# Performance work log

Measured on AMD Instinct MI355X. Metric: run time of the kernel, lower is better.

## Reference

```python
import jax, jax.numpy as jnp
import numpy as np

H = 128          # hidden_size
EF = 2           # expansion_factor
E = H * EF       # expanded hidden size
K = 4            # conv kernel size
R = 8            # dt_rank = ceil(128/16)
L = 2            # num_layers
BATCH = 2
SEQ = 1024
EPS = 1e-5


def rmsnorm(x, w):
    return x * jax.lax.rsqrt(jnp.mean(x * x, axis=-1, keepdims=True) + EPS) * w


def causal_conv1d(x, w, b):
    # x: (b, l, E); w: (E, 1, K) depthwise; left-pad K-1 => causal, output len l
    xt = jnp.transpose(x, (0, 2, 1))  # (b, E, l)
    out = jax.lax.conv_general_dilated(
        xt, w, window_strides=(1,), padding=[(K - 1, 0)],
        dimension_numbers=("NCH", "OIH", "NCH"), feature_group_count=E)
    out = out + b[None, :, None]
    return jnp.transpose(out, (0, 2, 1))


def sscan(xc, delta, A, Bm, Cm, Dp):
    # xc, delta: (b,l,E); A: (E,n); Bm, Cm: (b,l,n); Dp: (E,)
    deltaA = jnp.exp(jnp.einsum('bld,dn->bldn', delta, A))          # (b,l,E,n)
    deltaBx = jnp.einsum('bld,bln,bld->bldn', delta, Bm, xc)        # (b,l,E,n)

    def step(h, inp):
        dA_t, dBx_t, C_t = inp           # (b,E,n), (b,E,n), (b,n)
        h = dA_t * h + dBx_t
        y = jnp.einsum('bdn,bn->bd', h, C_t)
        return h, y

    b = xc.shape[0]
    h0 = jnp.zeros((b, E, A.shape[1]), dtype=xc.dtype)
    _, ys = jax.lax.scan(
        step, h0,
        (jnp.transpose(deltaA, (1, 0, 2, 3)),
         jnp.transpose(deltaBx, (1, 0, 2, 3)),
         jnp.transpose(Cm, (1, 0, 2))))
    y = jnp.transpose(ys, (1, 0, 2))     # (b,l,E)
    return y + Dp * xc


def mamba_block(x, in_w, in_b, out_w, out_b, pl_w, pl_b, dt_w, dt_b,
                conv_w, conv_b, A_log, Dp):
    xz = x @ in_w + in_b                 # (b,l,2E)
    xc, skip = jnp.split(xz, [E], axis=-1)
    xc = jax.nn.silu(causal_conv1d(xc, conv_w, conv_b))
    # ssm
    A = -jnp.exp(A_log)                  # (E,H)
    dbc = xc @ pl_w + pl_b               # (b,l,R+2H)
    delta, Bm, Cm = jnp.split(dbc, [R, R + H], axis=-1)
    delta = jax.nn.softplus(delta @ dt_w + dt_b)   # (b,l,E)
    y = sscan(xc, delta, A, Bm, Cm, Dp)
    y = y * jax.nn.silu(skip)
    return y @ out_w + out_b


def forward(x, in_w, in_b, out_w, out_b, pl_w, pl_b, dt_w, dt_b,
            conv_w, conv_b, A_log, Dp, norm_w, final_norm_w):
    for i in range(L):
        x = mamba_block(rmsnorm(x, norm_w[i]), in_w[i], in_b[i], out_w[i],
                        out_b[i], pl_w[i], pl_b[i], dt_w[i], dt_b[i],
                        conv_w[i], conv_b[i], A_log[i], Dp[i]) + x
    return rmsnorm(x, final_norm_w)


def setup_inputs() -> dict:
    key = jax.random.key(0)
    ks = jax.random.split(key, 12)
    s = 0.02
    x = jax.random.normal(ks[0], (BATCH, SEQ, H), dtype=jnp.float32)
    in_w = jax.random.normal(ks[1], (L, H, 2 * E)) * s
    in_b = jnp.zeros((L, 2 * E))
    out_w = jax.random.normal(ks[2], (L, E, H)) * s
    out_b = jnp.zeros((L, H))
    pl_w = jax.random.normal(ks[3], (L, E, R + 2 * H)) * s
    pl_b = jnp.zeros((L, R + 2 * H))
    dt_w = jax.random.normal(ks[4], (L, R, E)) * s
    dt_b = jnp.zeros((L, E))
    conv_w = jax.random.normal(ks[5], (L, E, 1, K)) * (1.0 / np.sqrt(K))
    conv_b = jnp.zeros((L, E))
    A_log = jnp.broadcast_to(jnp.log(jnp.arange(1, H + 1, dtype=jnp.float32)),
                             (L, E, H))
    Dp = jnp.ones((L, E))
    norm_w = jnp.ones((L, H))
    final_norm_w = jnp.ones((H,))
    return {"x": x, "in_w": in_w, "in_b": in_b, "out_w": out_w,
            "out_b": out_b, "pl_w": pl_w, "pl_b": pl_b, "dt_w": dt_w,
            "dt_b": dt_b, "conv_w": conv_w, "conv_b": conv_b,
            "A_log": A_log, "Dp": Dp, "norm_w": norm_w,
            "final_norm_w": final_norm_w}


def reference(x, in_w, in_b, out_w, out_b, pl_w, pl_b, dt_w, dt_b,
              conv_w, conv_b, A_log, Dp, norm_w, final_norm_w):
    return forward(x, in_w, in_b, out_w, out_b, pl_w, pl_b, dt_w, dt_b,
                   conv_w, conv_b, A_log, Dp, norm_w, final_norm_w)
```

## Files before the change

kernel.cpp:

```cpp
#include <hip/hip_runtime.h>
#include <hip/hip_bf16.h>

#define HH 128
#define EE 256
#define KK 4
#define RR 8
#define LL 2
#define BB 2
#define SS 1024
#define BT (BB*SS)
#define NJ (RR+2*HH)
#define GG 16
#define CH (SS/GG)
#define EPS 1e-5f
#define LOG2E 1.44269504088896f

__device__ __forceinline__ float silu_f(float v) {
    return v / (1.0f + __expf(-v));
}

__global__ __launch_bounds__(512) void k_norm_inproj(
    const float* __restrict__ xres, const float* __restrict__ inw,
    const float* __restrict__ inb, const float* __restrict__ nw,
    float* __restrict__ xz)
{
    __shared__ float xn[16][128];
    const int bt0 = blockIdx.x * 16;
    const int tid = threadIdx.x;
    {
        const int t = tid >> 5, g = tid & 31;
        const float4 xv = *(const float4*)(xres + (bt0 + t) * HH + g * 4);
        float ss = xv.x*xv.x + xv.y*xv.y + xv.z*xv.z + xv.w*xv.w;
        #pragma unroll
        for (int m = 16; m >= 1; m >>= 1) ss += __shfl_xor(ss, m);
        const float rs = rsqrtf(ss * (1.0f / HH) + EPS);
        const float4 wv = *(const float4*)(nw + g * 4);
        float4 o;
        o.x = xv.x * rs * wv.x; o.y = xv.y * rs * wv.y;
        o.z = xv.z * rs * wv.z; o.w = xv.w * rs * wv.w;
        *(float4*)(&xn[t][g * 4]) = o;
    }
    __syncthreads();
    const int j = tid;
    float acc[16];
    const float bj = inb[j];
    #pragma unroll
    for (int t = 0; t < 16; t++) acc[t] = bj;
    float w0n = inw[0*512 + j], w1n = inw[1*512 + j];
    float w2n = inw[2*512 + j], w3n = inw[3*512 + j];
    for (int k4 = 0; k4 < 32; k4++) {
        const float w0 = w0n, w1 = w1n, w2 = w2n, w3 = w3n;
        if (k4 < 31) {
            const int k = (k4 + 1) * 4;
            w0n = inw[(k+0)*512 + j]; w1n = inw[(k+1)*512 + j];
            w2n = inw[(k+2)*512 + j]; w3n = inw[(k+3)*512 + j];
        }
        const int k = k4 * 4;
        #pragma unroll
        for (int t = 0; t < 16; t++) {
            const float4 xv = *(const float4*)(&xn[t][k]);
            acc[t] += w0*xv.x + w1*xv.y + w2*xv.z + w3*xv.w;
        }
    }
    #pragma unroll
    for (int t = 0; t < 16; t++) xz[(bt0 + t) * 512 + j] = acc[t];
}

__global__ __launch_bounds__(256) void k_conv(
    const float* __restrict__ xz, const float* __restrict__ cw,
    const float* __restrict__ cb, float* __restrict__ xcT)
{
    const int e = threadIdx.x;
    const int tile = blockIdx.x;
    const int b = tile >> 6;
    const int t0 = (tile & 63) * 16;
    const float w0 = cw[e*4+0], w1 = cw[e*4+1], w2 = cw[e*4+2], w3 = cw[e*4+3];
    const float bias = cb[e];
    const float* xp = xz + (size_t)(b * SS) * 512 + e;
    float xm3 = (t0 >= 3) ? xp[(t0-3)*512] : 0.0f;
    float xm2 = (t0 >= 2) ? xp[(t0-2)*512] : 0.0f;
    float xm1 = (t0 >= 1) ? xp[(t0-1)*512] : 0.0f;
    float* orow = xcT + (size_t)e * BT + b * SS + t0;
    for (int jq = 0; jq < 4; jq++) {
        const int t = t0 + jq * 4;
        float4 ob; float v;
        const float x0 = xp[(t+0)*512];
        v = bias + w3*x0 + w2*xm1 + w1*xm2 + w0*xm3; ob.x = silu_f(v);
        const float x1 = xp[(t+1)*512];
        v = bias + w3*x1 + w2*x0 + w1*xm1 + w0*xm2;  ob.y = silu_f(v);
        const float x2 = xp[(t+2)*512];
        v = bias + w3*x2 + w2*x1 + w1*x0 + w0*xm1;   ob.z = silu_f(v);
        const float x3 = xp[(t+3)*512];
        v = bias + w3*x3 + w2*x2 + w1*x1 + w0*x0;    ob.w = silu_f(v);
        *(float4*)(orow + jq * 4) = ob;
        xm3 = x1; xm2 = x2; xm1 = x3;
    }
}

__global__ __launch_bounds__(320) void k_plproj(
    const float* __restrict__ xcT, const float* __restrict__ plw,
    const float* __restrict__ plb, float* __restrict__ dtrows,
    float* __restrict__ BC4)
{
    __shared__ float xs[8][256];
    const int bt0 = blockIdx.x * 8;
    const int tid = threadIdx.x;
    if (tid < 256) {
        const int e = tid;
        const float* p = xcT + (size_t)e * BT + bt0;
        const float4 a = *(const float4*)(p);
        const float4 c = *(const float4*)(p + 4);
        xs[0][e] = a.x; xs[1][e] = a.y; xs[2][e] = a.z; xs[3][e] = a.w;
        xs[4][e] = c.x; xs[5][e] = c.y; xs[6][e] = c.z; xs[7][e] = c.w;
    }
    __syncthreads();
    if (tid >= NJ) return;
    const int j = tid;
    float acc[8];
    const float bj = plb[j];
    #pragma unroll
    for (int t = 0; t < 8; t++) acc[t] = bj;
    float w0n = plw[0*NJ + j], w1n = plw[1*NJ + j];
    float w2n = plw[2*NJ + j], w3n = plw[3*NJ + j];
    for (int e4 = 0; e4 < 64; e4++) {
        const float w0 = w0n, w1 = w1n, w2 = w2n, w3 = w3n;
        if (e4 < 63) {
            const int e = (e4 + 1) * 4;
            w0n = plw[(e+0)*NJ + j]; w1n = plw[(e+1)*NJ + j];
            w2n = plw[(e+2)*NJ + j]; w3n = plw[(e+3)*NJ + j];
        }
        const int e = e4 * 4;
        #pragma unroll
        for (int t = 0; t < 8; t++) {
            const float4 xv = *(const float4*)(&xs[t][e]);
            acc[t] += w0*xv.x + w1*xv.y + w2*xv.z + w3*xv.w;
        }
    }
    if (j < RR) {
        float* orow = dtrows + (size_t)j * BT + bt0;
        *(float4*)(orow)     = make_float4(acc[0], acc[1], acc[2], acc[3]);
        *(float4*)(orow + 4) = make_float4(acc[4], acc[5], acc[6], acc[7]);
    } else {
        const int isC = (j >= RR + HH);
        const int nn = isC ? (j - RR - HH) : (j - RR);
        const int tq0 = bt0 >> 2;
        float* p0 = BC4 + ((size_t)tq0 * 128 + nn) * 8 + (isC ? 4 : 0);
        *(float4*)p0 = make_float4(acc[0], acc[1], acc[2], acc[3]);
        float* p1 = BC4 + ((size_t)(tq0 + 1) * 128 + nn) * 8 + (isC ? 4 : 0);
        *(float4*)p1 = make_float4(acc[4], acc[5], acc[6], acc[7]);
    }
}

__global__ __launch_bounds__(256) void k_delta(
    const float* __restrict__ dtrows, const float* __restrict__ dtw,
    const float* __restrict__ dtb, const float* __restrict__ xcT,
    float* __restrict__ deltaT, float* __restrict__ sT,
    float* __restrict__ dsum)
{
    const int e = blockIdx.x >> 3;
    const int bt = (blockIdx.x & 7) * 256 + threadIdx.x;
    float d = dtb[e];
    #pragma unroll
    for (int r = 0; r < RR; r++) d += dtw[r*EE + e] * dtrows[(size_t)r * BT + bt];
    float sp;
    if (d > 15.0f) sp = d;
    else sp = log1pf(__expf(d));
    const float xc = xcT[(size_t)e * BT + bt];
    deltaT[(size_t)e * BT + bt] = sp;
    sT[(size_t)e * BT + bt] = sp * xc;
    float cs = sp;
    #pragma unroll
    for (int m = 1; m <= 32; m <<= 1) cs += __shfl_xor(cs, m);
    if ((threadIdx.x & 63) == 0) {
        const int b = bt >> 10;
        const int g = (bt & 1023) >> 6;
        dsum[(b * EE + e) * GG + g] = cs;
    }
}

__global__ __launch_bounds__(128, 4) void k_scan_local(
    const float* __restrict__ BC4, const float* __restrict__ deltaT,
    const float* __restrict__ sT, const float* __restrict__ Alog,
    float* __restrict__ yT, float* __restrict__ hchain)
{
    __shared__ float part[2][16][68];
    __shared__ float ybuf[2][CH];
    const int blk = blockIdx.x;
    const int wgid = (blk & 7) * 512 + (blk >> 3);
    const int eq = wgid & 127;
    const int r0 = wgid >> 7;
    const int b = r0 >> 4;
    const int g = r0 & 15;
    const int e0 = eq * 2;
    const int n = threadIdx.x;
    const int t0 = g * CH;

    float An0 = -__expf(Alog[(e0+0) * HH + n]) * LOG2E;
    float An1 = -__expf(Alog[(e0+1) * HH + n]) * LOG2E;
    float h0 = 0.0f, h1 = 0.0f;
    const float* bc = BC4 + ((size_t)((b * 256 + g * 16) * 128 + n)) * 8;
    const float* dr0 = deltaT + (size_t)(e0+0) * BT + b * SS + t0;
    const float* dr1 = deltaT + (size_t)(e0+1) * BT + b * SS + t0;
    const float* sr0 = sT + (size_t)(e0+0) * BT + b * SS + t0;
    const float* sr1 = sT + (size_t)(e0+1) * BT + b * SS + t0;

    float4 pB = *(const float4*)(bc);
    float4 pC = *(const float4*)(bc + 4);
    float4 pd0 = *(const float4*)dr0, pd1 = *(const float4*)dr1;
    float4 ps0 = *(const float4*)sr0, ps1 = *(const float4*)sr1;

    const int tl = n >> 3, jj = n & 7;
    for (int sc = 0; sc < 4; sc++) {
        #pragma unroll
        for (int q = 0; q < 4; q++) {
            const int qq = sc * 4 + q;
            const float4 cB = pB, cC = pC;
            const float4 cd0 = pd0, cd1 = pd1, cs0 = ps0, cs1 = ps1;
            if (qq < 15) {
                const size_t off = (size_t)(qq + 1) * 1024;
                pB = *(const float4*)(bc + off);
                pC = *(const float4*)(bc + off + 4);
                const int t = (qq + 1) * 4;
                pd0 = *(const float4*)(dr0 + t); pd1 = *(const float4*)(dr1 + t);
                ps0 = *(const float4*)(sr0 + t); ps1 = *(const float4*)(sr1 + t);
            }
            float a;
            a = exp2f(cd0.x*An0); h0 = a*h0 + cs0.x*cB.x; part[0][q*4+0][n] = h0*cC.x;
            a = exp2f(cd0.y*An0); h0 = a*h0 + cs0.y*cB.y; part[0][q*4+1][n] = h0*cC.y;
            a = exp2f(cd0.z*An0); h0 = a*h0 + cs0.z*cB.z; part[0][q*4+2][n] = h0*cC.z;
            a = exp2f(cd0.w*An0); h0 = a*h0 + cs0.w*cB.w; part[0][q*4+3][n] = h0*cC.w;
            a = exp2f(cd1.x*An1); h1 = a*h1 + cs1.x*cB.x; part[1][q*4+0][n] = h1*cC.x;
            a = exp2f(cd1.y*An1); h1 = a*h1 + cs1.y*cB.y; part[1][q*4+1][n] = h1*cC.y;
            a = exp2f(cd1.z*An1); h1 = a*h1 + cs1.z*cB.z; part[1][q*4+2][n] = h1*cC.z;
            a = exp2f(cd1.w*An1); h1 = a*h1 + cs1.w*cB.w; part[1][q*4+3][n] = h1*cC.w;
        }
        __syncthreads();
        #pragma unroll
        for (int ee = 0; ee < 2; ee++) {
            float s0 = 0, s1 = 0, s2 = 0, s3 = 0;
            #pragma unroll
            for (int i = 0; i < 4; i++) {
                const float4 p = *(const float4*)(&part[ee][tl][jj*16 + i*4]);
                s0 += p.x; s1 += p.y; s2 += p.z; s3 += p.w;
            }
            float r = (s0 + s1) + (s2 + s3);
            r += __shfl_xor(r, 1); r += __shfl_xor(r, 2); r += __shfl_xor(r, 4);
            if (jj == 0) ybuf[ee][sc*16 + tl] = r;
        }
        __syncthreads();
    }
    {
        const int ee = n >> 6, tt = n & 63;
        yT[(size_t)(e0 + ee) * BT + b * SS + t0 + tt] = ybuf[ee][tt];
    }
    hchain[(size_t)(((b * EE + e0 + 0) * GG) + g) * 128 + n] = h0;
    hchain[(size_t)(((b * EE + e0 + 1) * GG) + g) * 128 + n] = h1;
}

__global__ __launch_bounds__(128) void k_scan_combine(
    const float* __restrict__ Alog, const float* __restrict__ dsum,
    float* __restrict__ hchain)
{
    const int be = blockIdx.x;
    const int e = be & 255;
    const int n = threadIdx.x;
    const float An = -__expf(Alog[e * HH + n]) * LOG2E;
    float h = 0.0f;
    for (int g = 0; g < GG; g++) {
        float* p = hchain + (size_t)(be * GG + g) * 128 + n;
        const float he = *p;
        *p = h;
        const float ds = dsum[be * GG + g];
        h = exp2f(An * ds) * h + he;
    }
}

__global__ __launch_bounds__(128, 4) void k_scan_fix(
    const float* __restrict__ BC4, const float* __restrict__ deltaT,
    const float* __restrict__ Alog, const float* __restrict__ hchain,
    float* __restrict__ yT)
{
    __shared__ float part[2][16][68];
    __shared__ float ybuf[2][CH];
    const int blk = blockIdx.x;
    const int wgid = (blk & 7) * 480 + (blk >> 3);
    const int eq = wgid & 127;
    const int r0 = wgid >> 7;
    const int b = r0 / 15;
    const int g = 1 + (r0 % 15);
    const int e0 = eq * 2;
    const int n = threadIdx.x;
    const int t0 = g * CH;

    const float An0 = -__expf(Alog[(e0+0) * HH + n]) * LOG2E;
    const float An1 = -__expf(Alog[(e0+1) * HH + n]) * LOG2E;
    const float w0 = hchain[(size_t)(((b * EE + e0 + 0) * GG) + g) * 128 + n];
    const float w1 = hchain[(size_t)(((b * EE + e0 + 1) * GG) + g) * 128 + n];
    float D0 = 0.0f, D1 = 0.0f;
    const float* bc = BC4 + ((size_t)((b * 256 + g * 16) * 128 + n)) * 8;
    const float* dr0 = deltaT + (size_t)(e0+0) * BT + b * SS + t0;
    const float* dr1 = deltaT + (size_t)(e0+1) * BT + b * SS + t0;

    float4 pC = *(const float4*)(bc + 4);
    float4 pd0 = *(const float4*)dr0, pd1 = *(const float4*)dr1;

    const int tl = n >> 3, jj = n & 7;
    for (int sc = 0; sc < 4; sc++) {
        #pragma unroll
        for (int q = 0; q < 4; q++) {
            const int qq = sc * 4 + q;
            const float4 cC = pC;
            const float4 cd0 = pd0, cd1 = pd1;
            if (qq < 15) {
                const size_t off = (size_t)(qq + 1) * 1024;
                pC = *(const float4*)(bc + off + 4);
                const int t = (qq + 1) * 4;
                pd0 = *(const float4*)(dr0 + t); pd1 = *(const float4*)(dr1 + t);
            }
            D0 += cd0.x; part[0][q*4+0][n] = exp2f(An0*D0) * w0 * cC.x;
            D0 += cd0.y; part[0][q*4+1][n] = exp2f(An0*D0) * w0 * cC.y;
            D0 += cd0.z; part[0][q*4+2][n] = exp2f(An0*D0) * w0 * cC.z;
            D0 += cd0.w; part[0][q*4+3][n] = exp2f(An0*D0) * w0 * cC.w;
            D1 += cd1.x; part[1][q*4+0][n] = exp2f(An1*D1) * w1 * cC.x;
            D1 += cd1.y; part[1][q*4+1][n] = exp2f(An1*D1) * w1 * cC.y;
            D1 += cd1.z; part[1][q*4+2][n] = exp2f(An1*D1) * w1 * cC.z;
            D1 += cd1.w; part[1][q*4+3][n] = exp2f(An1*D1) * w1 * cC.w;
        }
        __syncthreads();
        #pragma unroll
        for (int ee = 0; ee < 2; ee++) {
            float s0 = 0, s1 = 0, s2 = 0, s3 = 0;
            #pragma unroll
            for (int i = 0; i < 4; i++) {
                const float4 p = *(const float4*)(&part[ee][tl][jj*16 + i*4]);
                s0 += p.x; s1 += p.y; s2 += p.z; s3 += p.w;
            }
            float r = (s0 + s1) + (s2 + s3);
            r += __shfl_xor(r, 1); r += __shfl_xor(r, 2); r += __shfl_xor(r, 4);
            if (jj == 0) ybuf[ee][sc*16 + tl] = r;
        }
        __syncthreads();
    }
    {
        const int ee = n >> 6, tt = n & 63;
        yT[(size_t)(e0 + ee) * BT + b * SS + t0 + tt] += ybuf[ee][tt];
    }
}

__global__ __launch_bounds__(256) void k_gate_outproj(
    const float* __restrict__ yT, const float* __restrict__ xcT,
    const float* __restrict__ xz, const float* __restrict__ Dp,
    const float* __restrict__ ow, const float* __restrict__ ob,
    float* __restrict__ xres)
{
    __shared__ float gs[16][256];
    __shared__ float part2[16][128];
    const int bt0 = blockIdx.x * 16;
    const int tid = threadIdx.x;
    {
        const int e = tid;
        const float dp = Dp[e];
        const float* yp = yT + (size_t)e * BT + bt0;
        const float* xp = xcT + (size_t)e * BT + bt0;
        #pragma unroll
        for (int tq = 0; tq < 4; tq++) {
            const float4 y4 = *(const float4*)(yp + tq * 4);
            const float4 x4 = *(const float4*)(xp + tq * 4);
            float sk;
            sk = xz[(size_t)(bt0 + tq*4 + 0) * 512 + 256 + e];
            gs[tq*4+0][e] = (y4.x + dp * x4.x) * silu_f(sk);
            sk = xz[(size_t)(bt0 + tq*4 + 1) * 512 + 256 + e];
            gs[tq*4+1][e] = (y4.y + dp * x4.y) * silu_f(sk);
            sk = xz[(size_t)(bt0 + tq*4 + 2) * 512 + 256 + e];
            gs[tq*4+2][e] = (y4.z + dp * x4.z) * silu_f(sk);
            sk = xz[(size_t)(bt0 + tq*4 + 3) * 512 + 256 + e];
            gs[tq*4+3][e] = (y4.w + dp * x4.w) * silu_f(sk);
        }
    }
    __syncthreads();
    const int j = tid & 127;
    const int kh = tid >> 7;
    float acc[16];
    #pragma unroll
    for (int t = 0; t < 16; t++) acc[t] = 0.0f;
    const int eb = kh * 128;
    float w0n = ow[(eb+0)*HH + j], w1n = ow[(eb+1)*HH + j];
    float w2n = ow[(eb+2)*HH + j], w3n = ow[(eb+3)*HH + j];
    for (int e4 = 0; e4 < 32; e4++) {
        const float w0 = w0n, w1 = w1n, w2 = w2n, w3 = w3n;
        if (e4 < 31) {
            const int e = eb + (e4 + 1) * 4;
            w0n = ow[(e+0)*HH + j]; w1n = ow[(e+1)*HH + j];
            w2n = ow[(e+2)*HH + j]; w3n = ow[(e+3)*HH + j];
        }
        const int e = eb + e4 * 4;
        #pragma unroll
        for (int t = 0; t < 16; t++) {
            const float4 g4 = *(const float4*)(&gs[t][e]);
            acc[t] += w0*g4.x + w1*g4.y + w2*g4.z + w3*g4.w;
        }
    }
    if (kh == 1) {
        #pragma unroll
        for (int t = 0; t < 16; t++) part2[t][j] = acc[t];
    }
    __syncthreads();
    if (kh == 0) {
        const float bj = ob[j];
        #pragma unroll
        for (int t = 0; t < 16; t++) {
            const float r = acc[t] + part2[t][j] + bj
                          + xres[(size_t)(bt0 + t) * HH + j];
            xres[(size_t)(bt0 + t) * HH + j] = r;
        }
    }
}

__global__ __launch_bounds__(64) void k_finalnorm(
    const float* __restrict__ xres, const float* __restrict__ fw,
    float* __restrict__ out)
{
    const int bt = blockIdx.x;
    const int tid = threadIdx.x;
    const float2 v = *(const float2*)(xres + (size_t)bt * HH + tid * 2);
    float ss = v.x*v.x + v.y*v.y;
    #pragma unroll
    for (int m = 32; m >= 1; m >>= 1) ss += __shfl_xor(ss, m);
    const float rs = rsqrtf(ss * (1.0f / HH) + EPS);
    const float2 w = *(const float2*)(fw + tid * 2);
    float2 o; o.x = v.x * rs * w.x; o.y = v.y * rs * w.y;
    *(float2*)(out + (size_t)bt * HH + tid * 2) = o;
}

extern "C" void kernel_launch(void* const* d_in, const int* in_sizes, int n_in,
                              void* d_out, int out_size, void* d_ws, size_t ws_size,
                              hipStream_t stream)
{
    const float* x      = (const float*)d_in[0];
    const float* in_w   = (const float*)d_in[1];
    const float* in_b   = (const float*)d_in[2];
    const float* out_w  = (const float*)d_in[3];
    const float* out_b  = (const float*)d_in[4];
    const float* pl_w   = (const float*)d_in[5];
    const float* pl_b   = (const float*)d_in[6];
    const float* dt_w   = (const float*)d_in[7];
    const float* dt_b   = (const float*)d_in[8];
    const float* conv_w = (const float*)d_in[9];
    const float* conv_b = (const float*)d_in[10];
    const float* A_log  = (const float*)d_in[11];
    const float* Dp     = (const float*)d_in[12];
    const float* norm_w = (const float*)d_in[13];
    const float* fnw    = (const float*)d_in[14];

    float* ws     = (float*)d_ws;
    float* xres   = ws;
    float* xz     = xres   + 262144;
    float* xcT    = xz     + 1048576;
    float* dtrows = xcT    + 524288;
    float* BC4    = dtrows + 16384;
    float* deltaT = BC4    + 524288;
    float* sT     = deltaT + 524288;
    float* yT     = sT     + 524288;
    float* hchain = yT     + 524288;
    float* dsum   = hchain + 1048576;

    hipMemcpyAsync(xres, x, (size_t)262144 * sizeof(float),
                   hipMemcpyDeviceToDevice, stream);

    for (int l = 0; l < LL; l++) {
        k_norm_inproj<<<BT/16, 512, 0, stream>>>(
            xres, in_w + (size_t)l*HH*2*EE, in_b + (size_t)l*2*EE,
            norm_w + (size_t)l*HH, xz);
        k_conv<<<128, 256, 0, stream>>>(
            xz, conv_w + (size_t)l*EE*KK, conv_b + (size_t)l*EE, xcT);
        k_plproj<<<BT/8, 320, 0, stream>>>(
            xcT, pl_w + (size_t)l*EE*NJ, pl_b + (size_t)l*NJ, dtrows, BC4);
        k_delta<<<EE*8, 256, 0, stream>>>(
            dtrows, dt_w + (size_t)l*RR*EE, dt_b + (size_t)l*EE, xcT,
            deltaT, sT, dsum);
        k_scan_local<<<BB*GG*(EE/2), 128, 0, stream>>>(
            BC4, deltaT, sT, A_log + (size_t)l*EE*HH, yT, hchain);
        k_scan_combine<<<BB*EE, 128, 0, stream>>>(
            A_log + (size_t)l*EE*HH, dsum, hchain);
        k_scan_fix<<<BB*(GG-1)*(EE/2), 128, 0, stream>>>(
            BC4, deltaT, A_log + (size_t)l*EE*HH, hchain, yT);
        k_gate_outproj<<<BT/16, 256, 0, stream>>>(
            yT, xcT, xz, Dp + (size_t)l*EE,
            out_w + (size_t)l*EE*HH, out_b + (size_t)l*HH, xres);
    }
    k_finalnorm<<<BT, 64, 0, stream>>>(xres, fnw, (float*)d_out);
}
```

Before: 248.7 us.

## Fuse conv/projection/delta, fold scan combine into fix, fuse gate with next-layer inproj

Merges the conv, x_proj and delta/softplus kernels into one kernel that keeps the conv output in shared memory, so the dtrows buffer and its round trip disappear. The per-chunk delta sums are now accumulated inside the local scan, and each fix block rebuilds its carry-in state serially from hchain, which removes the separate combine kernel. The gate/out-projection kernel is templated so it also applies the next layer's RMSNorm and in-projection, or the final norm, and the initial device-to-device copy is dropped. Together these cut the per-forward launch count and intermediate memory traffic. The price is fewer, heavier blocks per fused kernel (less parallelism) and redundant serial carry recomputation in the fix blocks.

Result: slower. 267.1 us (+7.4%).

```diff
diff --git a/kernel.cpp b/kernel.cpp
--- a/kernel.cpp
+++ b/kernel.cpp
@@ -20,7 +20,7 @@
 }
 
 __global__ __launch_bounds__(512) void k_norm_inproj(
-    const float* __restrict__ xres, const float* __restrict__ inw,
+    const float* __restrict__ xin, const float* __restrict__ inw,
     const float* __restrict__ inb, const float* __restrict__ nw,
     float* __restrict__ xz)
 {
@@ -29,7 +29,7 @@
     const int tid = threadIdx.x;
     {
         const int t = tid >> 5, g = tid & 31;
-        const float4 xv = *(const float4*)(xres + (bt0 + t) * HH + g * 4);
+        const float4 xv = *(const float4*)(xin + (bt0 + t) * HH + g * 4);
         float ss = xv.x*xv.x + xv.y*xv.y + xv.z*xv.z + xv.w*xv.w;
         #pragma unroll
         for (int m = 16; m >= 1; m >>= 1) ss += __shfl_xor(ss, m);
@@ -66,122 +66,115 @@
     for (int t = 0; t < 16; t++) xz[(bt0 + t) * 512 + j] = acc[t];
 }
 
-__global__ __launch_bounds__(256) void k_conv(
+__global__ __launch_bounds__(512) void k_fused_cpd(
     const float* __restrict__ xz, const float* __restrict__ cw,
-    const float* __restrict__ cb, float* __restrict__ xcT)
+    const float* __restrict__ cb, const float* __restrict__ plw,
+    const float* __restrict__ plb, const float* __restrict__ dtw,
+    const float* __restrict__ dtb,
+    float* __restrict__ xcT, float* __restrict__ BC4,
+    float* __restrict__ deltaT, float* __restrict__ sT)
 {
-    const int e = threadIdx.x;
-    const int tile = blockIdx.x;
-    const int b = tile >> 6;
-    const int t0 = (tile & 63) * 16;
-    const float w0 = cw[e*4+0], w1 = cw[e*4+1], w2 = cw[e*4+2], w3 = cw[e*4+3];
-    const float bias = cb[e];
-    const float* xp = xz + (size_t)(b * SS) * 512 + e;
-    float xm3 = (t0 >= 3) ? xp[(t0-3)*512] : 0.0f;
-    float xm2 = (t0 >= 2) ? xp[(t0-2)*512] : 0.0f;
-    float xm1 = (t0 >= 1) ? xp[(t0-1)*512] : 0.0f;
-    float* orow = xcT + (size_t)e * BT + b * SS + t0;
-    for (int jq = 0; jq < 4; jq++) {
-        const int t = t0 + jq * 4;
-        float4 ob; float v;
-        const float x0 = xp[(t+0)*512];
-        v = bias + w3*x0 + w2*xm1 + w1*xm2 + w0*xm3; ob.x = silu_f(v);
-        const float x1 = xp[(t+1)*512];
-        v = bias + w3*x1 + w2*x0 + w1*xm1 + w0*xm2;  ob.y = silu_f(v);
-        const float x2 = xp[(t+2)*512];
-        v = bias + w3*x2 + w2*x1 + w1*x0 + w0*xm1;   ob.z = silu_f(v);
-        const float x3 = xp[(t+3)*512];
-        v = bias + w3*x3 + w2*x2 + w1*x1 + w0*x0;    ob.w = silu_f(v);
-        *(float4*)(orow + jq * 4) = ob;
-        xm3 = x1; xm2 = x2; xm1 = x3;
-    }
-}
-
-__global__ __launch_bounds__(320) void k_plproj(
-    const float* __restrict__ xcT, const float* __restrict__ plw,
-    const float* __restrict__ plb, float* __restrict__ dtrows,
-    float* __restrict__ BC4)
-{
-    __shared__ float xs[8][256];
-    const int bt0 = blockIdx.x * 8;
+    __shared__ float xcb[16][256];
+    __shared__ float dbc[8][16];
+    const int bt0 = blockIdx.x * 16;
     const int tid = threadIdx.x;
-    if (tid < 256) {
-        const int e = tid;
-        const float* p = xcT + (size_t)e * BT + bt0;
-        const float4 a = *(const float4*)(p);
-        const float4 c = *(const float4*)(p + 4);
-        xs[0][e] = a.x; xs[1][e] = a.y; xs[2][e] = a.z; xs[3][e] = a.w;
-        xs[4][e] = c.x; xs[5][e] = c.y; xs[6][e] = c.z; xs[7][e] = c.w;
+    {
+        const int e = tid & 255, hf = tid >> 8;
+        const int ts = bt0 + hf * 8;
+        const float w0 = cw[e*4+0], w1 = cw[e*4+1], w2 = cw[e*4+2], w3 = cw[e*4+3];
+        const float bias = cb[e];
+        const float* xp = xz + (size_t)ts * 512 + e;
+        const bool first = ((ts & 1023) == 0);
+        float xm3 = first ? 0.0f : xp[-3*512];
+        float xm2 = first ? 0.0f : xp[-2*512];
+        float xm1 = first ? 0.0f : xp[-1*512];
+        float xcv[8];
+        #pragma unroll
+        for (int i = 0; i < 8; i++) {
+            const float x0 = xp[i*512];
+            const float v = bias + w3*x0 + w2*xm1 + w1*xm2 + w0*xm3;
+            const float o = silu_f(v);
+            xcv[i] = o;
+            xcb[hf*8 + i][e] = o;
+            xm3 = xm2; xm2 = xm1; xm1 = x0;
+        }
+        float* orow = xcT + (size_t)e * BT + ts;
+        *(float4*)(orow)     = make_float4(xcv[0], xcv[1], xcv[2], xcv[3]);
+        *(float4*)(orow + 4) = make_float4(xcv[4], xcv[5], xcv[6], xcv[7]);
     }
     __syncthreads();
-    if (tid >= NJ) return;
-    const int j = tid;
-    float acc[8];
-    const float bj = plb[j];
-    #pragma unroll
-    for (int t = 0; t < 8; t++) acc[t] = bj;
-    float w0n = plw[0*NJ + j], w1n = plw[1*NJ + j];
-    float w2n = plw[2*NJ + j], w3n = plw[3*NJ + j];
-    for (int e4 = 0; e4 < 64; e4++) {
-        const float w0 = w0n, w1 = w1n, w2 = w2n, w3 = w3n;
-        if (e4 < 63) {
-            const int e = (e4 + 1) * 4;
-            w0n = plw[(e+0)*NJ + j]; w1n = plw[(e+1)*NJ + j];
-            w2n = plw[(e+2)*NJ + j]; w3n = plw[(e+3)*NJ + j];
-        }
-        const int e = e4 * 4;
-        #pragma unroll
-        for (int t = 0; t < 8; t++) {
-            const float4 xv = *(const float4*)(&xs[t][e]);
-            acc[t] += w0*xv.x + w1*xv.y + w2*xv.z + w3*xv.w;
-        }
-    }
-    if (j < RR) {
-        float* orow = dtrows + (size_t)j * BT + bt0;
-        *(float4*)(orow)     = make_float4(acc[0], acc[1], acc[2], acc[3]);
-        *(float4*)(orow + 4) = make_float4(acc[4], acc[5], acc[6], acc[7]);
-    } else {
-        const int isC = (j >= RR + HH);
-        const int nn = isC ? (j - RR - HH) : (j - RR);
-        const int tq0 = bt0 >> 2;
-        float* p0 = BC4 + ((size_t)tq0 * 128 + nn) * 8 + (isC ? 4 : 0);
-        *(float4*)p0 = make_float4(acc[0], acc[1], acc[2], acc[3]);
-        float* p1 = BC4 + ((size_t)(tq0 + 1) * 128 + nn) * 8 + (isC ? 4 : 0);
-        *(float4*)p1 = make_float4(acc[4], acc[5], acc[6], acc[7]);
-    }
-}
-
-__global__ __launch_bounds__(256) void k_delta(
-    const float* __restrict__ dtrows, const float* __restrict__ dtw,
-    const float* __restrict__ dtb, const float* __restrict__ xcT,
-    float* __restrict__ deltaT, float* __restrict__ sT,
-    float* __restrict__ dsum)
-{
-    const int e = blockIdx.x >> 3;
-    const int bt = (blockIdx.x & 7) * 256 + threadIdx.x;
-    float d = dtb[e];
-    #pragma unroll
-    for (int r = 0; r < RR; r++) d += dtw[r*EE + e] * dtrows[(size_t)r * BT + bt];
-    float sp;
-    if (d > 15.0f) sp = d;
-    else sp = log1pf(__expf(d));
-    const float xc = xcT[(size_t)e * BT + bt];
-    deltaT[(size_t)e * BT + bt] = sp;
-    sT[(size_t)e * BT + bt] = sp * xc;
-    float cs = sp;
-    #pragma unroll
-    for (int m = 1; m <= 32; m <<= 1) cs += __shfl_xor(cs, m);
-    if ((threadIdx.x & 63) == 0) {
-        const int b = bt >> 10;
-        const int g = (bt & 1023) >> 6;
-        dsum[(b * EE + e) * GG + g] = cs;
+    if (tid < NJ) {
+        const int j = tid;
+        float acc[16];
+        const float bj = plb[j];
+        #pragma unroll
+        for (int t = 0; t < 16; t++) acc[t] = bj;
+        float w0n = plw[0*NJ + j], w1n = plw[1*NJ + j];
+        float w2n = plw[2*NJ + j], w3n = plw[3*NJ + j];
+        for (int e4 = 0; e4 < 64; e4++) {
+            const float w0 = w0n, w1 = w1n, w2 = w2n, w3 = w3n;
+            if (e4 < 63) {
+                const int e = (e4 + 1) * 4;
+                w0n = plw[(e+0)*NJ + j]; w1n = plw[(e+1)*NJ + j];
+                w2n = plw[(e+2)*NJ + j]; w3n = plw[(e+3)*NJ + j];
+            }
+            const int e = e4 * 4;
+            #pragma unroll
+            for (int t = 0; t < 16; t++) {
+                const float4 xv = *(const float4*)(&xcb[t][e]);
+                acc[t] += w0*xv.x + w1*xv.y + w2*xv.z + w3*xv.w;
+            }
+        }
+        if (j < RR) {
+            #pragma unroll
+            for (int t = 0; t < 16; t++) dbc[j][t] = acc[t];
+        } else {
+            const int isC = (j >= RR + HH);
+            const int nn = isC ? (j - RR - HH) : (j - RR);
+            const int tq0 = bt0 >> 2;
+            #pragma unroll
+            for (int q = 0; q < 4; q++) {
+                float* p = BC4 + ((size_t)(tq0 + q) * 128 + nn) * 8 + (isC ? 4 : 0);
+                *(float4*)p = make_float4(acc[q*4+0], acc[q*4+1], acc[q*4+2], acc[q*4+3]);
+            }
+        }
+    }
+    __syncthreads();
+    {
+        const int e = tid & 255, hf = tid >> 8;
+        const int ts = bt0 + hf * 8;
+        float dv[8];
+        const float db = dtb[e];
+        #pragma unroll
+        for (int i = 0; i < 8; i++) dv[i] = db;
+        #pragma unroll
+        for (int r = 0; r < RR; r++) {
+            const float w = dtw[r*EE + e];
+            #pragma unroll
+            for (int i = 0; i < 8; i++) dv[i] += w * dbc[r][hf*8 + i];
+        }
+        float spv[8], sv[8];
+        #pragma unroll
+        for (int i = 0; i < 8; i++) {
+            const float d = dv[i];
+            const float sp = (d > 15.0f) ? d : log1pf(__expf(d));
+            spv[i] = sp;
+            sv[i] = sp * xcb[hf*8 + i][e];
+        }
+        float* drp = deltaT + (size_t)e * BT + ts;
+        *(float4*)(drp)     = make_float4(spv[0], spv[1], spv[2], spv[3]);
+        *(float4*)(drp + 4) = make_float4(spv[4], spv[5], spv[6], spv[7]);
+        float* srp = sT + (size_t)e * BT + ts;
+        *(float4*)(srp)     = make_float4(sv[0], sv[1], sv[2], sv[3]);
+        *(float4*)(srp + 4) = make_float4(sv[4], sv[5], sv[6], sv[7]);
     }
 }
 
 __global__ __launch_bounds__(128, 4) void k_scan_local(
     const float* __restrict__ BC4, const float* __restrict__ deltaT,
     const float* __restrict__ sT, const float* __restrict__ Alog,
-    float* __restrict__ yT, float* __restrict__ hchain)
+    float* __restrict__ yT, float* __restrict__ hchain,
+    float* __restrict__ dsum)
 {
     __shared__ float part[2][16][68];
     __shared__ float ybuf[2][CH];
@@ -197,7 +190,7 @@
 
     float An0 = -__expf(Alog[(e0+0) * HH + n]) * LOG2E;
     float An1 = -__expf(Alog[(e0+1) * HH + n]) * LOG2E;
-    float h0 = 0.0f, h1 = 0.0f;
+    float h0 = 0.0f, h1 = 0.0f, cum0 = 0.0f, cum1 = 0.0f;
     const float* bc = BC4 + ((size_t)((b * 256 + g * 16) * 128 + n)) * 8;
     const float* dr0 = deltaT + (size_t)(e0+0) * BT + b * SS + t0;
     const float* dr1 = deltaT + (size_t)(e0+1) * BT + b * SS + t0;
@@ -233,6 +226,8 @@
             a = exp2f(cd1.y*An1); h1 = a*h1 + cs1.y*cB.y; part[1][q*4+1][n] = h1*cC.y;
             a = exp2f(cd1.z*An1); h1 = a*h1 + cs1.z*cB.z; part[1][q*4+2][n] = h1*cC.z;
             a = exp2f(cd1.w*An1); h1 = a*h1 + cs1.w*cB.w; part[1][q*4+3][n] = h1*cC.w;
+            cum0 += (cd0.x + cd0.y) + (cd0.z + cd0.w);
+            cum1 += (cd1.x + cd1.y) + (cd1.z + cd1.w);
         }
         __syncthreads();
         #pragma unroll
@@ -255,30 +250,16 @@
     }
     hchain[(size_t)(((b * EE + e0 + 0) * GG) + g) * 128 + n] = h0;
     hchain[(size_t)(((b * EE + e0 + 1) * GG) + g) * 128 + n] = h1;
-}
-
-__global__ __launch_bounds__(128) void k_scan_combine(
-    const float* __restrict__ Alog, const float* __restrict__ dsum,
-    float* __restrict__ hchain)
-{
-    const int be = blockIdx.x;
-    const int e = be & 255;
-    const int n = threadIdx.x;
-    const float An = -__expf(Alog[e * HH + n]) * LOG2E;
-    float h = 0.0f;
-    for (int g = 0; g < GG; g++) {
-        float* p = hchain + (size_t)(be * GG + g) * 128 + n;
-        const float he = *p;
-        *p = h;
-        const float ds = dsum[be * GG + g];
-        h = exp2f(An * ds) * h + he;
+    if (n == 0) {
+        dsum[(b * EE + e0 + 0) * GG + g] = cum0;
+        dsum[(b * EE + e0 + 1) * GG + g] = cum1;
     }
 }
 
 __global__ __launch_bounds__(128, 4) void k_scan_fix(
     const float* __restrict__ BC4, const float* __restrict__ deltaT,
     const float* __restrict__ Alog, const float* __restrict__ hchain,
-    float* __restrict__ yT)
+    const float* __restrict__ dsum, float* __restrict__ yT)
 {
     __shared__ float part[2][16][68];
     __shared__ float ybuf[2][CH];
@@ -294,8 +275,19 @@
 
     const float An0 = -__expf(Alog[(e0+0) * HH + n]) * LOG2E;
     const float An1 = -__expf(Alog[(e0+1) * HH + n]) * LOG2E;
-    const float w0 = hchain[(size_t)(((b * EE + e0 + 0) * GG) + g) * 128 + n];
-    const float w1 = hchain[(size_t)(((b * EE + e0 + 1) * GG) + g) * 128 + n];
+    float w0 = 0.0f, w1 = 0.0f;
+    {
+        const size_t hb0 = (size_t)((b * EE + e0 + 0) * GG) * 128 + n;
+        const size_t hb1 = (size_t)((b * EE + e0 + 1) * GG) * 128 + n;
+        const int db0 = (b * EE + e0 + 0) * GG;
+        const int db1 = (b * EE + e0 + 1) * GG;
+        for (int gp = 0; gp < g; gp++) {
+            const float he0 = hchain[hb0 + (size_t)gp * 128];
+            const float he1 = hchain[hb1 + (size_t)gp * 128];
+            w0 = exp2f(An0 * dsum[db0 + gp]) * w0 + he0;
+            w1 = exp2f(An1 * dsum[db1 + gp]) * w1 + he1;
+        }
+    }
     float D0 = 0.0f, D1 = 0.0f;
     const float* bc = BC4 + ((size_t)((b * 256 + g * 16) * 128 + n)) * 8;
     const float* dr0 = deltaT + (size_t)(e0+0) * BT + b * SS + t0;
@@ -347,14 +339,18 @@
     }
 }
 
-__global__ __launch_bounds__(256) void k_gate_outproj(
+template<int NEXT, int FINAL>
+__global__ __launch_bounds__(256) void k_gate(
     const float* __restrict__ yT, const float* __restrict__ xcT,
     const float* __restrict__ xz, const float* __restrict__ Dp,
     const float* __restrict__ ow, const float* __restrict__ ob,
-    float* __restrict__ xres)
+    const float* __restrict__ resin, float* __restrict__ xres,
+    const float* __restrict__ nw, const float* __restrict__ inw,
+    const float* __restrict__ inb, float* __restrict__ xznext,
+    const float* __restrict__ fw, float* __restrict__ out)
 {
     __shared__ float gs[16][256];
-    __shared__ float part2[16][128];
+    __shared__ float rb[16][132];
     const int bt0 = blockIdx.x * 16;
     const int tid = threadIdx.x;
     {
@@ -380,56 +376,95 @@
     __syncthreads();
     const int j = tid & 127;
     const int kh = tid >> 7;
-    float acc[16];
-    #pragma unroll
-    for (int t = 0; t < 16; t++) acc[t] = 0.0f;
-    const int eb = kh * 128;
-    float w0n = ow[(eb+0)*HH + j], w1n = ow[(eb+1)*HH + j];
-    float w2n = ow[(eb+2)*HH + j], w3n = ow[(eb+3)*HH + j];
-    for (int e4 = 0; e4 < 32; e4++) {
-        const float w0 = w0n, w1 = w1n, w2 = w2n, w3 = w3n;
-        if (e4 < 31) {
-            const int e = eb + (e4 + 1) * 4;
-            w0n = ow[(e+0)*HH + j]; w1n = ow[(e+1)*HH + j];
-            w2n = ow[(e+2)*HH + j]; w3n = ow[(e+3)*HH + j];
-        }
-        const int e = eb + e4 * 4;
+    {
+        float acc[16];
+        #pragma unroll
+        for (int t = 0; t < 16; t++) acc[t] = 0.0f;
+        const int eb = kh * 128;
+        float w0n = ow[(eb+0)*HH + j], w1n = ow[(eb+1)*HH + j];
+        float w2n = ow[(eb+2)*HH + j], w3n = ow[(eb+3)*HH + j];
+        for (int e4 = 0; e4 < 32; e4++) {
+            const float w0 = w0n, w1 = w1n, w2 = w2n, w3 = w3n;
+            if (e4 < 31) {
+                const int e = eb + (e4 + 1) * 4;
+                w0n = ow[(e+0)*HH + j]; w1n = ow[(e+1)*HH + j];
+                w2n = ow[(e+2)*HH + j]; w3n = ow[(e+3)*HH + j];
+            }
+            const int e = eb + e4 * 4;
+            #pragma unroll
+            for (int t = 0; t < 16; t++) {
+                const float4 g4 = *(const float4*)(&gs[t][e]);
+                acc[t] += w0*g4.x + w1*g4.y + w2*g4.z + w3*g4.w;
+            }
+        }
+        if (kh == 1) {
+            #pragma unroll
+            for (int t = 0; t < 16; t++) rb[t][j] = acc[t];
+        }
+        __syncthreads();
+        if (kh == 0) {
+            const float bj = ob[j];
+            #pragma unroll
+            for (int t = 0; t < 16; t++) {
+                const float r = acc[t] + rb[t][j] + bj
+                              + resin[(size_t)(bt0 + t) * HH + j];
+                if (!FINAL) xres[(size_t)(bt0 + t) * HH + j] = r;
+                rb[t][j] = r;
+            }
+        }
+    }
+    if (NEXT || FINAL) {
+        __syncthreads();
+        const int t = tid >> 4, g16 = tid & 15;
+        const float4 a = *(const float4*)(&rb[t][g16*8]);
+        const float4 c = *(const float4*)(&rb[t][g16*8 + 4]);
+        float ss = a.x*a.x + a.y*a.y + a.z*a.z + a.w*a.w
+                 + c.x*c.x + c.y*c.y + c.z*c.z + c.w*c.w;
+        ss += __shfl_xor(ss, 1); ss += __shfl_xor(ss, 2);
+        ss += __shfl_xor(ss, 4); ss += __shfl_xor(ss, 8);
+        if (g16 == 0) rb[t][128] = rsqrtf(ss * (1.0f / HH) + EPS);
+        __syncthreads();
+    }
+    if (FINAL) {
+        const int jc = tid & 127, th = tid >> 7;
+        const float fwj = fw[jc];
+        #pragma unroll
+        for (int i = 0; i < 8; i++) {
+            const int t = th * 8 + i;
+            out[(size_t)(bt0 + t) * HH + jc] = rb[t][jc] * rb[t][128] * fwj;
+        }
+    }
+    if (NEXT) {
+        const int j0 = tid, j1 = tid + 256;
+        float acc0[16], acc1[16];
+        #pragma unroll
+        for (int t = 0; t < 16; t++) { acc0[t] = 0.0f; acc1[t] = 0.0f; }
+        for (int k4 = 0; k4 < 32; k4++) {
+            const int k = k4 * 4;
+            const float4 nv = *(const float4*)(nw + k);
+            const float u0 = inw[(k+0)*512 + j0] * nv.x;
+            const float u1 = inw[(k+1)*512 + j0] * nv.y;
+            const float u2 = inw[(k+2)*512 + j0] * nv.z;
+            const float u3 = inw[(k+3)*512 + j0] * nv.w;
+            const float v0 = inw[(k+0)*512 + j1] * nv.x;
+            const float v1 = inw[(k+1)*512 + j1] * nv.y;
+            const float v2 = inw[(k+2)*512 + j1] * nv.z;
+            const float v3 = inw[(k+3)*512 + j1] * nv.w;
+            #pragma unroll
+            for (int t = 0; t < 16; t++) {
+                const float4 xv = *(const float4*)(&rb[t][k]);
+                acc0[t] += u0*xv.x + u1*xv.y + u2*xv.z + u3*xv.w;
+                acc1[t] += v0*xv.x + v1*xv.y + v2*xv.z + v3*xv.w;
+            }
+        }
+        const float b0 = inb[j0], b1 = inb[j1];
         #pragma unroll
         for (int t = 0; t < 16; t++) {
-            const float4 g4 = *(const float4*)(&gs[t][e]);
-            acc[t] += w0*g4.x + w1*g4.y + w2*g4.z + w3*g4.w;
-        }
-    }
-    if (kh == 1) {
-        #pragma unroll
-        for (int t = 0; t < 16; t++) part2[t][j] = acc[t];
-    }
-    __syncthreads();
-    if (kh == 0) {
-        const float bj = ob[j];
-        #pragma unroll
-        for (int t = 0; t < 16; t++) {
-            const float r = acc[t] + part2[t][j] + bj
-                          + xres[(size_t)(bt0 + t) * HH + j];
-            xres[(size_t)(bt0 + t) * HH + j] = r;
-        }
-    }
-}
-
-__global__ __launch_bounds__(64) void k_finalnorm(
-    const float* __restrict__ xres, const float* __restrict__ fw,
-    float* __restrict__ out)
-{
-    const int bt = blockIdx.x;
-    const int tid = threadIdx.x;
-    const float2 v = *(const float2*)(xres + (size_t)bt * HH + tid * 2);
-    float ss = v.x*v.x + v.y*v.y;
-    #pragma unroll
-    for (int m = 32; m >= 1; m >>= 1) ss += __shfl_xor(ss, m);
-    const float rs = rsqrtf(ss * (1.0f / HH) + EPS);
-    const float2 w = *(const float2*)(fw + tid * 2);
-    float2 o; o.x = v.x * rs * w.x; o.y = v.y * rs * w.y;
-    *(float2*)(out + (size_t)bt * HH + tid * 2) = o;
+            const float rs = rb[t][128];
+            xznext[(size_t)(bt0 + t) * 512 + j0] = acc0[t] * rs + b0;
+            xznext[(size_t)(bt0 + t) * 512 + j1] = acc1[t] * rs + b1;
+        }
+    }
 }
 
 extern "C" void kernel_launch(void* const* d_in, const int* in_sizes, int n_in,
@@ -456,37 +491,34 @@
     float* xres   = ws;
     float* xz     = xres   + 262144;
     float* xcT    = xz     + 1048576;
-    float* dtrows = xcT    + 524288;
-    float* BC4    = dtrows + 16384;
+    float* BC4    = xcT    + 524288;
     float* deltaT = BC4    + 524288;
     float* sT     = deltaT + 524288;
     float* yT     = sT     + 524288;
     float* hchain = yT     + 524288;
     float* dsum   = hchain + 1048576;
 
-    hipMemcpyAsync(xres, x, (size_t)262144 * sizeof(float),
-                   hipMemcpyDeviceToDevice, stream);
-
-    for (int l = 0; l < LL; l++) {
-        k_norm_inproj<<<BT/16, 512, 0, stream>>>(
-            xres, in_w + (size_t)l*HH*2*EE, in_b + (size_t)l*2*EE,
-            norm_w + (size_t)l*HH, xz);
-        k_conv<<<128, 256, 0, stream>>>(
-            xz, conv_w + (size_t)l*EE*KK, conv_b + (size_t)l*EE, xcT);
-        k_plproj<<<BT/8, 320, 0, stream>>>(
-            xcT, pl_w + (size_t)l*EE*NJ, pl_b + (size_t)l*NJ, dtrows, BC4);
-        k_delta<<<EE*8, 256, 0, stream>>>(
-            dtrows, dt_w + (size_t)l*RR*EE, dt_b + (size_t)l*EE, xcT,
-            deltaT, sT, dsum);
-        k_scan_local<<<BB*GG*(EE/2), 128, 0, stream>>>(
-            BC4, deltaT, sT, A_log + (size_t)l*EE*HH, yT, hchain);
-        k_scan_combine<<<BB*EE, 128, 0, stream>>>(
-            A_log + (size_t)l*EE*HH, dsum, hchain);
-        k_scan_fix<<<BB*(GG-1)*(EE/2), 128, 0, stream>>>(
-            BC4, deltaT, A_log + (size_t)l*EE*HH, hchain, yT);
-        k_gate_outproj<<<BT/16, 256, 0, stream>>>(
-            yT, xcT, xz, Dp + (size_t)l*EE,
-            out_w + (size_t)l*EE*HH, out_b + (size_t)l*HH, xres);
-    }
-    k_finalnorm<<<BT, 64, 0, stream>>>(xres, fnw, (float*)d_out);
-}
+    k_norm_inproj<<<BT/16, 512, 0, stream>>>(x, in_w, in_b, norm_w, xz);
+    k_fused_cpd<<<BT/16, 512, 0, stream>>>(
+        xz, conv_w, conv_b, pl_w, pl_b, dt_w, dt_b, xcT, BC4, deltaT, sT);
+    k_scan_local<<<BB*GG*(EE/2), 128, 0, stream>>>(
+        BC4, deltaT, sT, A_log, yT, hchain, dsum);
+    k_scan_fix<<<BB*(GG-1)*(EE/2), 128, 0, stream>>>(
+        BC4, deltaT, A_log, hchain, dsum, yT);
+    k_gate<1, 0><<<BT/16, 256, 0, stream>>>(
+        yT, xcT, xz, Dp, out_w, out_b, x, xres,
+        norm_w + HH, in_w + (size_t)HH*2*EE, in_b + 2*EE, xz,
+        nullptr, nullptr);
+
+    k_fused_cpd<<<BT/16, 512, 0, stream>>>(
+        xz, conv_w + EE*KK, conv_b + EE, pl_w + (size_t)EE*NJ, pl_b + NJ,
+        dt_w + RR*EE, dt_b + EE, xcT, BC4, deltaT, sT);
+    k_scan_local<<<BB*GG*(EE/2), 128, 0, stream>>>(
+        BC4, deltaT, sT, A_log + (size_t)EE*HH, yT, hchain, dsum);
+    k_scan_fix<<<BB*(GG-1)*(EE/2), 128, 0, stream>>>(
+        BC4, deltaT, A_log + (size_t)EE*HH, hchain, dsum, yT);
+    k_gate<0, 1><<<BT/16, 256, 0, stream>>>(
+        yT, xcT, xz, Dp + EE, out_w + (size_t)EE*HH, out_b + HH, xres, xres,
+        nullptr, nullptr, nullptr, nullptr,
+        fnw, (float*)d_out);
+}
```
